# Optimization experiments

Measured on AMD Instinct MI355X. Metric: run time of the kernel, lower is better.

## Reference

```python
import jax, jax.numpy as jnp
import numpy as np

B, N, E = 2, 20000, 640000
FREL_DIMS = [16, 128, 64, 32, 16, 16]   # rel_in_dim -> ... -> 16 (message dim)
FDYN_DIMS = [30, 128, 64, 32, 16, 6]    # (dyn_in_dim=14 + 16) -> ... -> delta_dim=6


def _mlp(x, params):
    # FourLayerMLP: Linear+ReLU x4, final Linear (no activation)
    for w, b in params[:-1]:
        x = jax.nn.relu(x @ w + b)
    w, b = params[-1]
    return x @ w + b


def setup_inputs() -> dict:
    key = jax.random.key(0)
    ks = jax.random.split(key, 16)
    inp = {
        "dyn": jax.random.normal(ks[0], (B, N, 14), jnp.float32),
        "rel": jax.random.normal(ks[1], (B, E, 16), jnp.float32),
        "send": jax.random.randint(ks[2], (E,), 0, N, dtype=jnp.int64),
        "recv": jax.random.randint(ks[3], (E,), 0, N, dtype=jnp.int64),
    }
    ki = 4
    for name, dims in (("frel", FREL_DIMS), ("fdyn", FDYN_DIMS)):
        for li in range(5):
            inp[f"{name}_w{li}"] = 0.05 * jax.random.normal(ks[ki], (dims[li], dims[li + 1]), jnp.float32)
            inp[f"{name}_b{li}"] = jnp.zeros((dims[li + 1],), jnp.float32)
            ki += 1
    return inp


def reference(dyn, rel, send, recv,
              frel_w0, frel_b0, frel_w1, frel_b1, frel_w2, frel_b2,
              frel_w3, frel_b3, frel_w4, frel_b4,
              fdyn_w0, fdyn_b0, fdyn_w1, fdyn_b1, fdyn_w2, fdyn_b2,
              fdyn_w3, fdyn_b3, fdyn_w4, fdyn_b4):
    frel = [(frel_w0, frel_b0), (frel_w1, frel_b1), (frel_w2, frel_b2),
            (frel_w3, frel_b3), (frel_w4, frel_b4)]
    fdyn = [(fdyn_w0, fdyn_b0), (fdyn_w1, fdyn_b1), (fdyn_w2, fdyn_b2),
            (fdyn_w3, fdyn_b3), (fdyn_w4, fdyn_b4)]
    b, n, _ = dyn.shape
    msg = _mlp(rel, frel)                                      # [B, E, 16]
    # index_add_ over node dim, recv shared across batch
    agg = jnp.zeros((b, n, 16), dyn.dtype).at[:, recv].add(msg)  # [B, N, 16]
    return _mlp(jnp.concatenate([dyn, agg], axis=-1), fdyn)    # [B, N, 6]
```

## Files before the change

### kernel.cpp

```cpp
#include <hip/hip_runtime.h>
#include <hip/hip_bf16.h>

#define BB 2
#define NN 20000
#define EE 640000

using short8 = __attribute__((ext_vector_type(8))) short;
using f32x4  = __attribute__((ext_vector_type(4))) float;
typedef unsigned int uint;

__device__ __forceinline__ uint b16u(float x) {
    return (uint)__bfloat16_as_ushort(__float2bfloat16(x));
}
__device__ __forceinline__ void split2(float x, float y, uint& hi, uint& lo) {
    const uint hx = b16u(x), hy = b16u(y);
    hi = hx | (hy << 16);
    const float fx = __uint_as_float(hx << 16), fy = __uint_as_float(hy << 16);
    lo = b16u(x - fx) | (b16u(y - fy) << 16);
}

template<int KT>
__device__ __forceinline__ void loadB(const char* H, const char* L, int rowb, int emask,
                                      int li, int q, short8* bh, short8* bl) {
    const int sw = (li & emask) << 4;
    const char* rh = H + li * rowb;
    const char* rl = L + li * rowb;
#pragma unroll
    for (int kt = 0; kt < KT; ++kt) {
        const int off = (kt * 64 + q * 16) ^ sw;
        bh[kt] = *(const short8*)(rh + off);
        bl[kt] = *(const short8*)(rl + off);
    }
}

#define MFMA16(a, b, c) __builtin_amdgcn_mfma_f32_16x16x32_bf16(a, b, c, 0, 0, 0)

template<int KT, int MT, int WOFF>
__device__ __forceinline__ void layer_r(const short8 (&wh)[30], const short8 (&wl)[30],
                                        const float* bias, int q,
                                        const short8* bh, const short8* bl, f32x4* acc) {
#pragma unroll
    for (int mt = 0; mt < MT; ++mt) {
        const float4 bv = *(const float4*)(bias + mt * 16 + q * 4);
        acc[mt][0] = bv.x; acc[mt][1] = bv.y; acc[mt][2] = bv.z; acc[mt][3] = bv.w;
    }
#pragma unroll
    for (int kt = 0; kt < KT; ++kt) {
#pragma unroll
        for (int mt = 0; mt < MT; ++mt) acc[mt] = MFMA16(wh[WOFF + mt * KT + kt], bh[kt], acc[mt]);
#pragma unroll
        for (int mt = 0; mt < MT; ++mt) acc[mt] = MFMA16(wh[WOFF + mt * KT + kt], bl[kt], acc[mt]);
#pragma unroll
        for (int mt = 0; mt < MT; ++mt) acc[mt] = MFMA16(wl[WOFF + mt * KT + kt], bh[kt], acc[mt]);
    }
}

template<int MT>
__device__ __forceinline__ void store_acts(char* H, char* L, int rowb, int emask,
                                           int lane, const f32x4* acc) {
    const int li = lane & 15, q = lane >> 4;
    const int sw = (li & emask) << 4;
    char* rh = H + li * rowb;
    char* rl = L + li * rowb;
#pragma unroll
    for (int mt = 0; mt < MT; ++mt) {
        const float v0 = fmaxf(acc[mt][0], 0.f), v1 = fmaxf(acc[mt][1], 0.f);
        const float v2 = fmaxf(acc[mt][2], 0.f), v3 = fmaxf(acc[mt][3], 0.f);
        uint h01, l01, h23, l23;
        split2(v0, v1, h01, l01);
        split2(v2, v3, h23, l23);
        const int off = (mt * 32 + q * 8) ^ sw;
        *(uint*)(rh + off) = h01; *(uint*)(rh + off + 4) = h23;
        *(uint*)(rl + off) = l01; *(uint*)(rl + off + 4) = l23;
    }
}

__device__ __forceinline__ void stage16(char* H, char* L, int se, int sc, float4 v) {
    uint h01, l01, h23, l23;
    split2(v.x, v.y, h01, l01);
    split2(v.z, v.w, h23, l23);
    const int sw = (se & 7) << 4;
    char* rh = H + se * 128; char* rl = L + se * 128;
    const int o = (sc * 8) ^ sw;
    *(uint*)(rh + o) = h01; *(uint*)(rh + o + 4) = h23;
    *(uint*)(rl + o) = l01; *(uint*)(rl + o + 4) = l23;
    const int oz = (32 + sc * 8) ^ sw;
    *(uint*)(rh + oz) = 0; *(uint*)(rh + oz + 4) = 0;
    *(uint*)(rl + oz) = 0; *(uint*)(rl + oz + 4) = 0;
}

__device__ __forceinline__ void padX2(char* H, char* L, int li, int q) {
    const int sw = (li & 7) << 4;
    const int oz = (32 + q * 8) ^ sw;
    *(uint*)(H + li * 128 + oz) = 0; *(uint*)(H + li * 128 + oz + 4) = 0;
    *(uint*)(L + li * 128 + oz) = 0; *(uint*)(L + li * 128 + oz + 4) = 0;
}

template<int CSR>
__global__ __launch_bounds__(64, 1) void edge_mlp2(
    const float* __restrict__ rel, const int* __restrict__ recv, const int* __restrict__ posOf,
    const char* __restrict__ wfrag,
    const float* __restrict__ b0, const float* __restrict__ b1, const float* __restrict__ b2,
    const float* __restrict__ b3, const float* __restrict__ b4,
    float* __restrict__ outp) {
    __shared__ __align__(16) char XA0H[16 * 128], XA0L[16 * 128];
    __shared__ __align__(16) char XA1H[16 * 256], XA1L[16 * 256];
    __shared__ __align__(16) char XA2H[16 * 128], XA2L[16 * 128];
    __shared__ __align__(16) char XB0H[16 * 128], XB0L[16 * 128];
    __shared__ __align__(16) char XB1H[16 * 256], XB1L[16 * 256];
    __shared__ __align__(16) char XB2H[16 * 128], XB2L[16 * 128];
    __shared__ __align__(16) float BIAS[256];

    const int lane = threadIdx.x;
    const int li = lane & 15, q = lane >> 4;
    const int se = lane >> 2, sc = lane & 3;

    if (lane < 32)      *(float4*)&BIAS[lane * 4] = *(const float4*)(b0 + lane * 4);
    else if (lane < 48) *(float4*)&BIAS[128 + (lane - 32) * 4] = *(const float4*)(b1 + (lane - 32) * 4);
    else if (lane < 56) *(float4*)&BIAS[192 + (lane - 48) * 4] = *(const float4*)(b2 + (lane - 48) * 4);
    else if (lane < 60) *(float4*)&BIAS[224 + (lane - 56) * 4] = *(const float4*)(b3 + (lane - 56) * 4);
    else                *(float4*)&BIAS[240 + (lane - 60) * 4] = *(const float4*)(b4 + (lane - 60) * 4);

    short8 wh[30], wl[30];
#pragma unroll
    for (int f = 0; f < 30; ++f) {
        const char* pp = wfrag + (size_t)f * 2048 + lane * 16;
        wh[f] = *(const short8*)pp;
        wl[f] = *(const short8*)(pp + 1024);
    }

    constexpr int PPB = EE / 16;
    constexpr int NPAIR = BB * PPB / 2;
    const int G = gridDim.x;

    int pr = blockIdx.x;
    if (pr >= NPAIR) return;

    float4 rvA, rvB; int ixA, ixB;
    {
        const int pA = 2 * pr;
        const int bb = pA / PPB, e0 = (pA % PPB) * 16;
        rvA = *(const float4*)(rel + ((size_t)bb * EE + e0 + se) * 16 + sc * 4);
        rvB = *(const float4*)(rel + ((size_t)bb * EE + e0 + 16 + se) * 16 + sc * 4);
        ixA = CSR ? posOf[e0 + li] : recv[e0 + li];
        ixB = CSR ? posOf[e0 + 16 + li] : recv[e0 + 16 + li];
    }

    while (true) {
        const int pA = 2 * pr;
        const int bA = pA / PPB;
        const int prn = pr + G;
        const bool more = prn < NPAIR;
        float4 rnA = {0.f, 0.f, 0.f, 0.f}, rnB = {0.f, 0.f, 0.f, 0.f};
        int jxA = 0, jxB = 0;
        if (more) {
            const int pN = 2 * prn;
            const int bb = pN / PPB, e0 = (pN % PPB) * 16;
            rnA = *(const float4*)(rel + ((size_t)bb * EE + e0 + se) * 16 + sc * 4);
            rnB = *(const float4*)(rel + ((size_t)bb * EE + e0 + 16 + se) * 16 + sc * 4);
            jxA = CSR ? posOf[e0 + li] : recv[e0 + li];
            jxB = CSR ? posOf[e0 + 16 + li] : recv[e0 + 16 + li];
        }

        stage16(XA0H, XA0L, se, sc, rvA);
        stage16(XB0H, XB0L, se, sc, rvB);

        short8 bhA[4], blA[4], bhB[4], blB[4];
        f32x4 aA[8], aB[8];

        loadB<1>(XA0H, XA0L, 128, 7, li, q, bhA, blA);
        loadB<1>(XB0H, XB0L, 128, 7, li, q, bhB, blB);
        layer_r<1, 8, 0>(wh, wl, BIAS + 0, q, bhA, blA, aA);
        store_acts<8>(XA1H, XA1L, 256, 7, lane, aA);
        layer_r<1, 8, 0>(wh, wl, BIAS + 0, q, bhB, blB, aB);
        store_acts<8>(XB1H, XB1L, 256, 7, lane, aB);
        loadB<4>(XA1H, XA1L, 256, 7, li, q, bhA, blA);
        loadB<4>(XB1H, XB1L, 256, 7, li, q, bhB, blB);
        layer_r<4, 4, 8>(wh, wl, BIAS + 128, q, bhA, blA, aA);
        store_acts<4>(XA2H, XA2L, 128, 7, lane, aA);
        layer_r<4, 4, 8>(wh, wl, BIAS + 128, q, bhB, blB, aB);
        store_acts<4>(XB2H, XB2L, 128, 7, lane, aB);
        loadB<2>(XA2H, XA2L, 128, 7, li, q, bhA, blA);
        loadB<2>(XB2H, XB2L, 128, 7, li, q, bhB, blB);
        layer_r<2, 2, 24>(wh, wl, BIAS + 192, q, bhA, blA, aA);
        store_acts<2>(XA0H, XA0L, 128, 7, lane, aA);
        layer_r<2, 2, 24>(wh, wl, BIAS + 192, q, bhB, blB, aB);
        store_acts<2>(XB0H, XB0L, 128, 7, lane, aB);
        loadB<1>(XA0H, XA0L, 128, 7, li, q, bhA, blA);
        loadB<1>(XB0H, XB0L, 128, 7, li, q, bhB, blB);
        layer_r<1, 1, 28>(wh, wl, BIAS + 224, q, bhA, blA, aA);
        store_acts<1>(XA2H, XA2L, 128, 7, lane, aA);
        layer_r<1, 1, 28>(wh, wl, BIAS + 224, q, bhB, blB, aB);
        store_acts<1>(XB2H, XB2L, 128, 7, lane, aB);
        padX2(XA2H, XA2L, li, q);
        padX2(XB2H, XB2L, li, q);
        loadB<1>(XA2H, XA2L, 128, 7, li, q, bhA, blA);
        loadB<1>(XB2H, XB2L, 128, 7, li, q, bhB, blB);
        layer_r<1, 1, 29>(wh, wl, BIAS + 240, q, bhA, blA, aA);
        layer_r<1, 1, 29>(wh, wl, BIAS + 240, q, bhB, blB, aB);

        if (CSR) {
            float4 vA, vB;
            vA.x = aA[0][0]; vA.y = aA[0][1]; vA.z = aA[0][2]; vA.w = aA[0][3];
            vB.x = aB[0][0]; vB.y = aB[0][1]; vB.z = aB[0][2]; vB.w = aB[0][3];
            *(float4*)(outp + ((size_t)bA * EE + ixA) * 16 + q * 4) = vA;
            *(float4*)(outp + ((size_t)bA * EE + ixB) * 16 + q * 4) = vB;
        } else {
            float* dA = outp + ((size_t)bA * NN + ixA) * 16 + q * 4;
            atomicAdd(dA + 0, aA[0][0]); atomicAdd(dA + 1, aA[0][1]);
            atomicAdd(dA + 2, aA[0][2]); atomicAdd(dA + 3, aA[0][3]);
            float* dB = outp + ((size_t)bA * NN + ixB) * 16 + q * 4;
            atomicAdd(dB + 0, aB[0][0]); atomicAdd(dB + 1, aB[0][1]);
            atomicAdd(dB + 2, aB[0][2]); atomicAdd(dB + 3, aB[0][3]);
        }
        if (!more) break;
        pr = prn; rvA = rnA; rvB = rnB; ixA = jxA; ixB = jxB;
    }
}

__global__ __launch_bounds__(64, 1) void node_mlp_r(
    const float* __restrict__ dyn, const float* __restrict__ agg,
    const char* __restrict__ wfrag,
    const float* __restrict__ b0, const float* __restrict__ b1, const float* __restrict__ b2,
    const float* __restrict__ b3, const float* __restrict__ b4,
    float* __restrict__ out) {
    __shared__ __align__(16) char XH0[16 * 128], XL0[16 * 128];
    __shared__ __align__(16) char XH1[16 * 256], XL1[16 * 256];
    __shared__ __align__(16) char XH2[16 * 128], XL2[16 * 128];
    __shared__ __align__(16) float BIAS[256];

    const int lane = threadIdx.x;
    const int li = lane & 15, q = lane >> 4;

    if (lane < 32)      *(float4*)&BIAS[lane * 4] = *(const float4*)(b0 + lane * 4);
    else if (lane < 48) *(float4*)&BIAS[128 + (lane - 32) * 4] = *(const float4*)(b1 + (lane - 32) * 4);
    else if (lane < 56) *(float4*)&BIAS[192 + (lane - 48) * 4] = *(const float4*)(b2 + (lane - 48) * 4);
    else if (lane < 60) *(float4*)&BIAS[224 + (lane - 56) * 4] = *(const float4*)(b3 + (lane - 56) * 4);
    else if (lane == 60) *(float4*)&BIAS[240] = *(const float4*)(b4);
    else if (lane == 61) { BIAS[244] = b4[4]; BIAS[245] = b4[5]; BIAS[246] = 0.f; BIAS[247] = 0.f; }
    else { BIAS[248 + (lane - 62) * 4] = 0.f; BIAS[249 + (lane - 62) * 4] = 0.f;
           BIAS[250 + (lane - 62) * 4] = 0.f; BIAS[251 + (lane - 62) * 4] = 0.f; }

    short8 wh[30], wl[30];
#pragma unroll
    for (int f = 0; f < 30; ++f) {
        const char* pp = wfrag + 61440 + (size_t)f * 2048 + lane * 16;
        wh[f] = *(const short8*)pp;
        wl[f] = *(const short8*)(pp + 1024);
    }

    constexpr int NPN = BB * (NN / 16);
    for (int p = blockIdx.x; p < NPN; p += gridDim.x) {
        const int b = p / (NN / 16);
        const int ng0 = (p % (NN / 16)) * 16;
        {
            const int n = lane >> 2, p4 = lane & 3;
            const size_t dbase = ((size_t)b * NN + ng0 + n) * 14;
            const size_t abase = ((size_t)b * NN + ng0 + n) * 16;
            float qa0, qa1, qa2, qa3, qb0, qb1, qb2, qb3;
            if (p4 < 3) {
                const float2 u = *(const float2*)(dyn + dbase + 4 * p4);
                const float2 w = *(const float2*)(dyn + dbase + 4 * p4 + 2);
                qa0 = u.x; qa1 = u.y; qa2 = w.x; qa3 = w.y;
                const float2 g0 = *(const float2*)(agg + abase + 2 + 4 * p4);
                const float2 g1 = *(const float2*)(agg + abase + 4 + 4 * p4);
                qb0 = g0.x; qb1 = g0.y; qb2 = g1.x; qb3 = g1.y;
            } else {
                const float2 u = *(const float2*)(dyn + dbase + 12);
                const float2 g = *(const float2*)(agg + abase + 0);
                qa0 = u.x; qa1 = u.y; qa2 = g.x; qa3 = g.y;
                const float2 g2 = *(const float2*)(agg + abase + 14);
                qb0 = g2.x; qb1 = g2.y; qb2 = 0.f; qb3 = 0.f;
            }
            const int sw = (n & 7) << 4;
            char* rh = XH0 + n * 128; char* rl = XL0 + n * 128;
            uint h01, l01, h23, l23;
            split2(qa0, qa1, h01, l01);
            split2(qa2, qa3, h23, l23);
            const int o = (p4 * 8) ^ sw;
            *(uint*)(rh + o) = h01; *(uint*)(rh + o + 4) = h23;
            *(uint*)(rl + o) = l01; *(uint*)(rl + o + 4) = l23;
            split2(qb0, qb1, h01, l01);
            split2(qb2, qb3, h23, l23);
            const int o2 = (32 + p4 * 8) ^ sw;
            *(uint*)(rh + o2) = h01; *(uint*)(rh + o2 + 4) = h23;
            *(uint*)(rl + o2) = l01; *(uint*)(rl + o2 + 4) = l23;
        }
        short8 bh[4], bl[4];
        f32x4 acc[8];

        loadB<1>(XH0, XL0, 128, 7, li, q, bh, bl);
        layer_r<1, 8, 0>(wh, wl, BIAS + 0, q, bh, bl, acc);
        store_acts<8>(XH1, XL1, 256, 7, lane, acc);

        loadB<4>(XH1, XL1, 256, 7, li, q, bh, bl);
        layer_r<4, 4, 8>(wh, wl, BIAS + 128, q, bh, bl, acc);
        store_acts<4>(XH2, XL2, 128, 7, lane, acc);

        loadB<2>(XH2, XL2, 128, 7, li, q, bh, bl);
        layer_r<2, 2, 24>(wh, wl, BIAS + 192, q, bh, bl, acc);
        store_acts<2>(XH0, XL0, 128, 7, lane, acc);

        loadB<1>(XH0, XL0, 128, 7, li, q, bh, bl);
        layer_r<1, 1, 28>(wh, wl, BIAS + 224, q, bh, bl, acc);
        store_acts<1>(XH2, XL2, 128, 7, lane, acc);
        padX2(XH2, XL2, li, q);

        loadB<1>(XH2, XL2, 128, 7, li, q, bh, bl);
        layer_r<1, 1, 29>(wh, wl, BIAS + 240, q, bh, bl, acc);

        const int gn = ng0 + li;
#pragma unroll
        for (int r = 0; r < 4; ++r) {
            const int ch = q * 4 + r;
            if (ch < 6) out[((size_t)b * NN + gn) * 6 + ch] = acc[0][r];
        }
    }
}

__global__ __launch_bounds__(64) void wprep(
    const float* w0f, const float* w1f, const float* w2f, const float* w3f, const float* w4f,
    const float* w0d, const float* w1d, const float* w2d, const float* w3d, const float* w4d,
    char* __restrict__ wfrag) {
    const int bid = blockIdx.x;
    const int lane = threadIdx.x;
    const int net = bid / 30;
    const int r = bid % 30;
    int l, base;
    if (r < 8)       { l = 0; base = 0; }
    else if (r < 24) { l = 1; base = 8; }
    else if (r < 28) { l = 2; base = 24; }
    else if (r < 29) { l = 3; base = 28; }
    else             { l = 4; base = 29; }
    const int KTs[5] = {1, 4, 2, 1, 1};
    const int Krf[5] = {16, 128, 64, 32, 16};
    const int Krd[5] = {30, 128, 64, 32, 16};
    const int Ncf[5] = {128, 64, 32, 16, 16};
    const int Ncd[5] = {128, 64, 32, 16, 6};
    const float* Wf[5] = {w0f, w1f, w2f, w3f, w4f};
    const float* Wd[5] = {w0d, w1d, w2d, w3d, w4d};
    const int KT = KTs[l];
    const int idx = r - base;
    const int mt = idx / KT, kt = idx % KT;
    const int Kreal = net ? Krd[l] : Krf[l];
    const int Ncol  = net ? Ncd[l] : Ncf[l];
    const float* W  = net ? Wd[l] : Wf[l];
    const int ch = mt * 16 + (lane & 15);
    uint hi[4], lo[4];
#pragma unroll
    for (int t = 0; t < 4; ++t) {
        float x = 0.f, y = 0.f;
        const int k0 = kt * 32 + (lane >> 4) * 8 + 2 * t;
        if (k0 < Kreal && ch < Ncol) x = W[(size_t)k0 * Ncol + ch];
        if (k0 + 1 < Kreal && ch < Ncol) y = W[(size_t)(k0 + 1) * Ncol + ch];
        split2(x, y, hi[t], lo[t]);
    }
    uint4 H; H.x = hi[0]; H.y = hi[1]; H.z = hi[2]; H.w = hi[3];
    uint4 L; L.x = lo[0]; L.y = lo[1]; L.z = lo[2]; L.w = lo[3];
    *(uint4*)(wfrag + (size_t)bid * 2048 + lane * 16) = H;
    *(uint4*)(wfrag + (size_t)bid * 2048 + 1024 + lane * 16) = L;
}

__global__ void count_k(const int* __restrict__ recv, int* __restrict__ counts) {
    const int e = blockIdx.x * 256 + threadIdx.x;
    if (e < EE) atomicAdd(&counts[recv[e]], 1);
}

__global__ __launch_bounds__(1024) void scan_k(const int* __restrict__ counts,
                                               int* __restrict__ start, int* __restrict__ cursor) {
    __shared__ int part[1024];
    const int t = threadIdx.x;
    const int lo = t * 20, hi = lo + 20 < NN ? lo + 20 : NN;
    int s = 0;
    for (int i = lo; i < hi; ++i) s += counts[i];
    part[t] = s;
    __syncthreads();
    for (int d = 1; d < 1024; d <<= 1) {
        int v = 0;
        if (t >= d) v = part[t - d];
        __syncthreads();
        part[t] += v;
        __syncthreads();
    }
    int run = t ? part[t - 1] : 0;
    for (int i = lo; i < hi; ++i) { start[i] = run; cursor[i] = run; run += counts[i]; }
    if (t == 0) start[NN] = EE;
}

__global__ void fill_k(const int* __restrict__ recv, int* __restrict__ cursor,
                       int* __restrict__ posOf) {
    const int e = blockIdx.x * 256 + threadIdx.x;
    if (e < EE) posOf[e] = atomicAdd(&cursor[recv[e]], 1);
}

__global__ void gather_k(const float* __restrict__ msg, const int* __restrict__ start,
                         float* __restrict__ agg) {
    const int t = blockIdx.x * 256 + threadIdx.x;
    if (t >= BB * NN * 4) return;
    const int oq = t & 3;
    const int bn = t >> 2;
    const int n = bn % NN, b = bn / NN;
    const int s = start[n], e = start[n + 1];
    float4 S; S.x = 0.f; S.y = 0.f; S.z = 0.f; S.w = 0.f;
    for (int i = s; i < e; ++i) {
        const float4 v = *(const float4*)(msg + ((size_t)b * EE + i) * 16 + oq * 4);
        S.x += v.x; S.y += v.y; S.z += v.z; S.w += v.w;
    }
    *(float4*)(agg + (size_t)bn * 16 + oq * 4) = S;
}

extern "C" void kernel_launch(void* const* d_in, const int* in_sizes, int n_in,
                              void* d_out, int out_size, void* d_ws, size_t ws_size,
                              hipStream_t stream) {
    const float* dyn = (const float*)d_in[0];
    const float* rel = (const float*)d_in[1];
    const int* recv = (const int*)d_in[3];

    const float* fw[5]; const float* fb[5]; const float* dw[5]; const float* db[5];
    for (int i = 0; i < 5; ++i) {
        fw[i] = (const float*)d_in[4 + 2 * i];
        fb[i] = (const float*)d_in[5 + 2 * i];
        dw[i] = (const float*)d_in[14 + 2 * i];
        db[i] = (const float*)d_in[15 + 2 * i];
    }

    char* ws = (char*)d_ws;
    char* wfrag = ws;
    const size_t MSG_OFF = 131072;
    const size_t MSG_SZ = (size_t)BB * EE * 16 * 4;
    const size_t POS_OFF = MSG_OFF + MSG_SZ;
    const size_t CNT_OFF = POS_OFF + (size_t)EE * 4;
    const size_t CUR_OFF = CNT_OFF + (size_t)NN * 4;
    const size_t STA_OFF = CUR_OFF + (size_t)NN * 4;
    const size_t AGG_OFF_CSR = STA_OFF + 80128;
    const size_t NEED = AGG_OFF_CSR + (size_t)BB * NN * 16 * 4;
    const bool csr = ws_size >= NEED;

    wprep<<<60, 64, 0, stream>>>(fw[0], fw[1], fw[2], fw[3], fw[4],
                                 dw[0], dw[1], dw[2], dw[3], dw[4], wfrag);

    float* agg;
    if (csr) {
        float* msg = (float*)(ws + MSG_OFF);
        int* posOf = (int*)(ws + POS_OFF);
        int* counts = (int*)(ws + CNT_OFF);
        int* cursor = (int*)(ws + CUR_OFF);
        int* start = (int*)(ws + STA_OFF);
        agg = (float*)(ws + AGG_OFF_CSR);

        hipMemsetAsync(counts, 0, (size_t)NN * 4, stream);
        count_k<<<(EE + 255) / 256, 256, 0, stream>>>(recv, counts);
        scan_k<<<1, 1024, 0, stream>>>(counts, start, cursor);
        fill_k<<<(EE + 255) / 256, 256, 0, stream>>>(recv, cursor, posOf);
        edge_mlp2<1><<<2048, 64, 0, stream>>>(
            rel, recv, posOf, wfrag, fb[0], fb[1], fb[2], fb[3], fb[4], msg);
        gather_k<<<(BB * NN * 4 + 255) / 256, 256, 0, stream>>>(msg, start, agg);
    } else {
        agg = (float*)(ws + MSG_OFF);
        hipMemsetAsync(agg, 0, (size_t)BB * NN * 16 * 4, stream);
        edge_mlp2<0><<<2048, 64, 0, stream>>>(
            rel, recv, nullptr, wfrag, fb[0], fb[1], fb[2], fb[3], fb[4], agg);
    }

    node_mlp_r<<<1024, 64, 0, stream>>>(
        dyn, agg, wfrag, db[0], db[1], db[2], db[3], db[4], (float*)d_out);
}
```

Before: 471.2 us.

## Fuse CSR gather of edge messages into node MLP kernel

Removes the separate gather kernel and agg buffer. Each lane of the node MLP now sums its four message channels over its node's CSR edge range and feeds the sums straight into the layer-0 input. It also packs the bf16 hi/lo split with a paired conversion intrinsic. The aim is to save a launch and an agg write and read round trip. The cost is that the gather now runs inside a low-occupancy kernel (64 threads, one block per CU per launch bounds) with only 1024 blocks, so latency on the serial edge loops may be poorly hidden.

New measurement: 497.3 us. 5.5% more time.

```diff
diff --git a/kernel.cpp b/kernel.cpp
--- a/kernel.cpp
+++ b/kernel.cpp
@@ -9,14 +9,16 @@
 using f32x4  = __attribute__((ext_vector_type(4))) float;
 typedef unsigned int uint;
 
-__device__ __forceinline__ uint b16u(float x) {
-    return (uint)__bfloat16_as_ushort(__float2bfloat16(x));
+__device__ __forceinline__ uint pack_bf16x2(float x, float y) {
+    union { __hip_bfloat162 b; uint u; } c;
+    c.b = __float22bfloat162_rn(make_float2(x, y));
+    return c.u;
 }
 __device__ __forceinline__ void split2(float x, float y, uint& hi, uint& lo) {
-    const uint hx = b16u(x), hy = b16u(y);
-    hi = hx | (hy << 16);
-    const float fx = __uint_as_float(hx << 16), fy = __uint_as_float(hy << 16);
-    lo = b16u(x - fx) | (b16u(y - fy) << 16);
+    hi = pack_bf16x2(x, y);
+    const float fx = __uint_as_float(hi << 16);
+    const float fy = __uint_as_float(hi & 0xffff0000u);
+    lo = pack_bf16x2(x - fx, y - fy);
 }
 
 template<int KT>
@@ -218,8 +220,10 @@
     }
 }
 
+template<int CSR>
 __global__ __launch_bounds__(64, 1) void node_mlp_r(
-    const float* __restrict__ dyn, const float* __restrict__ agg,
+    const float* __restrict__ dyn, const float* __restrict__ msgOrAgg,
+    const int* __restrict__ start,
     const char* __restrict__ wfrag,
     const float* __restrict__ b0, const float* __restrict__ b1, const float* __restrict__ b2,
     const float* __restrict__ b3, const float* __restrict__ b4,
@@ -231,6 +235,7 @@
 
     const int lane = threadIdx.x;
     const int li = lane & 15, q = lane >> 4;
+    const int n4 = lane >> 2, p4 = lane & 3;
 
     if (lane < 32)      *(float4*)&BIAS[lane * 4] = *(const float4*)(b0 + lane * 4);
     else if (lane < 48) *(float4*)&BIAS[128 + (lane - 32) * 4] = *(const float4*)(b1 + (lane - 32) * 4);
@@ -249,31 +254,48 @@
         wl[f] = *(const short8*)(pp + 1024);
     }
 
+    const int co0 = (p4 < 3) ? 2 + 4 * p4 : 0;
+    const int co1 = (p4 < 3) ? 4 + 4 * p4 : 14;
+
     constexpr int NPN = BB * (NN / 16);
     for (int p = blockIdx.x; p < NPN; p += gridDim.x) {
         const int b = p / (NN / 16);
         const int ng0 = (p % (NN / 16)) * 16;
+        const int gn = ng0 + n4;
+
+        float g0, g1, g2, g3;
+        if (CSR) {
+            g0 = g1 = g2 = g3 = 0.f;
+            const int s = start[gn], e = start[gn + 1];
+            const float* mb = msgOrAgg + (size_t)b * EE * 16;
+            for (int i = s; i < e; ++i) {
+                const float* mp = mb + (size_t)i * 16;
+                const float2 u = *(const float2*)(mp + co0);
+                const float2 v = *(const float2*)(mp + co1);
+                g0 += u.x; g1 += u.y; g2 += v.x; g3 += v.y;
+            }
+        } else {
+            const size_t abase = ((size_t)b * NN + gn) * 16;
+            const float2 u = *(const float2*)(msgOrAgg + abase + co0);
+            const float2 v = *(const float2*)(msgOrAgg + abase + co1);
+            g0 = u.x; g1 = u.y; g2 = v.x; g3 = v.y;
+        }
+
         {
-            const int n = lane >> 2, p4 = lane & 3;
-            const size_t dbase = ((size_t)b * NN + ng0 + n) * 14;
-            const size_t abase = ((size_t)b * NN + ng0 + n) * 16;
+            const size_t dbase = ((size_t)b * NN + gn) * 14;
             float qa0, qa1, qa2, qa3, qb0, qb1, qb2, qb3;
             if (p4 < 3) {
                 const float2 u = *(const float2*)(dyn + dbase + 4 * p4);
                 const float2 w = *(const float2*)(dyn + dbase + 4 * p4 + 2);
                 qa0 = u.x; qa1 = u.y; qa2 = w.x; qa3 = w.y;
-                const float2 g0 = *(const float2*)(agg + abase + 2 + 4 * p4);
-                const float2 g1 = *(const float2*)(agg + abase + 4 + 4 * p4);
-                qb0 = g0.x; qb1 = g0.y; qb2 = g1.x; qb3 = g1.y;
+                qb0 = g0; qb1 = g1; qb2 = g2; qb3 = g3;
             } else {
                 const float2 u = *(const float2*)(dyn + dbase + 12);
-                const float2 g = *(const float2*)(agg + abase + 0);
-                qa0 = u.x; qa1 = u.y; qa2 = g.x; qa3 = g.y;
-                const float2 g2 = *(const float2*)(agg + abase + 14);
-                qb0 = g2.x; qb1 = g2.y; qb2 = 0.f; qb3 = 0.f;
+                qa0 = u.x; qa1 = u.y; qa2 = g0; qa3 = g1;
+                qb0 = g2; qb1 = g3; qb2 = 0.f; qb3 = 0.f;
             }
-            const int sw = (n & 7) << 4;
-            char* rh = XH0 + n * 128; char* rl = XL0 + n * 128;
+            const int sw = (n4 & 7) << 4;
+            char* rh = XH0 + n4 * 128; char* rl = XL0 + n4 * 128;
             uint h01, l01, h23, l23;
             split2(qa0, qa1, h01, l01);
             split2(qa2, qa3, h23, l23);
@@ -309,11 +331,11 @@
         loadB<1>(XH2, XL2, 128, 7, li, q, bh, bl);
         layer_r<1, 1, 29>(wh, wl, BIAS + 240, q, bh, bl, acc);
 
-        const int gn = ng0 + li;
+        const int on = ng0 + li;
 #pragma unroll
         for (int r = 0; r < 4; ++r) {
             const int ch = q * 4 + r;
-            if (ch < 6) out[((size_t)b * NN + gn) * 6 + ch] = acc[0][r];
+            if (ch < 6) out[((size_t)b * NN + on) * 6 + ch] = acc[0][r];
         }
     }
 }
@@ -393,22 +415,6 @@
     if (e < EE) posOf[e] = atomicAdd(&cursor[recv[e]], 1);
 }
 
-__global__ void gather_k(const float* __restrict__ msg, const int* __restrict__ start,
-                         float* __restrict__ agg) {
-    const int t = blockIdx.x * 256 + threadIdx.x;
-    if (t >= BB * NN * 4) return;
-    const int oq = t & 3;
-    const int bn = t >> 2;
-    const int n = bn % NN, b = bn / NN;
-    const int s = start[n], e = start[n + 1];
-    float4 S; S.x = 0.f; S.y = 0.f; S.z = 0.f; S.w = 0.f;
-    for (int i = s; i < e; ++i) {
-        const float4 v = *(const float4*)(msg + ((size_t)b * EE + i) * 16 + oq * 4);
-        S.x += v.x; S.y += v.y; S.z += v.z; S.w += v.w;
-    }
-    *(float4*)(agg + (size_t)bn * 16 + oq * 4) = S;
-}
-
 extern "C" void kernel_launch(void* const* d_in, const int* in_sizes, int n_in,
                               void* d_out, int out_size, void* d_ws, size_t ws_size,
                               hipStream_t stream) {
@@ -432,21 +438,18 @@
     const size_t CNT_OFF = POS_OFF + (size_t)EE * 4;
     const size_t CUR_OFF = CNT_OFF + (size_t)NN * 4;
     const size_t STA_OFF = CUR_OFF + (size_t)NN * 4;
-    const size_t AGG_OFF_CSR = STA_OFF + 80128;
-    const size_t NEED = AGG_OFF_CSR + (size_t)BB * NN * 16 * 4;
+    const size_t NEED = STA_OFF + 80128;
     const bool csr = ws_size >= NEED;
 
     wprep<<<60, 64, 0, stream>>>(fw[0], fw[1], fw[2], fw[3], fw[4],
                                  dw[0], dw[1], dw[2], dw[3], dw[4], wfrag);
 
-    float* agg;
     if (csr) {
         float* msg = (float*)(ws + MSG_OFF);
         int* posOf = (int*)(ws + POS_OFF);
         int* counts = (int*)(ws + CNT_OFF);
         int* cursor = (int*)(ws + CUR_OFF);
         int* start = (int*)(ws + STA_OFF);
-        agg = (float*)(ws + AGG_OFF_CSR);
 
         hipMemsetAsync(counts, 0, (size_t)NN * 4, stream);
         count_k<<<(EE + 255) / 256, 256, 0, stream>>>(recv, counts);
@@ -454,14 +457,14 @@
         fill_k<<<(EE + 255) / 256, 256, 0, stream>>>(recv, cursor, posOf);
         edge_mlp2<1><<<2048, 64, 0, stream>>>(
             rel, recv, posOf, wfrag, fb[0], fb[1], fb[2], fb[3], fb[4], msg);
-        gather_k<<<(BB * NN * 4 + 255) / 256, 256, 0, stream>>>(msg, start, agg);
+        node_mlp_r<1><<<1024, 64, 0, stream>>>(
+            dyn, msg, start, wfrag, db[0], db[1], db[2], db[3], db[4], (float*)d_out);
     } else {
-        agg = (float*)(ws + MSG_OFF);
+        float* agg = (float*)(ws + MSG_OFF);
         hipMemsetAsync(agg, 0, (size_t)BB * NN * 16 * 4, stream);
         edge_mlp2<0><<<2048, 64, 0, stream>>>(
             rel, recv, nullptr, wfrag, fb[0], fb[1], fb[2], fb[3], fb[4], agg);
-    }
-
-    node_mlp_r<<<1024, 64, 0, stream>>>(
-        dyn, agg, wfrag, db[0], db[1], db[2], db[3], db[4], (float*)d_out);
-}
+        node_mlp_r<0><<<1024, 64, 0, stream>>>(
+            dyn, agg, nullptr, wfrag, db[0], db[1], db[2], db[3], db[4], (float*)d_out);
+    }
+}
```
